# Kernel optimization log

Measured on AMD Instinct MI355X. Metric: run time of the kernel, lower is better.

Reference implementation:

```python
import jax, jax.numpy as jnp
import numpy as np

B, S, H = 16, 2048, 1024
NEG_INF = -10000000.0


def setup_inputs() -> dict:
    key = jax.random.key(0)
    ks = jax.random.split(key, 9)
    s = 1.0 / np.sqrt(H)
    return {
        "queries": jax.random.normal(ks[0], (B, S, H), jnp.float32),
        "keys": jax.random.normal(ks[1], (B, S, H), jnp.float32),
        "values": jax.random.normal(ks[2], (B, S, H), jnp.float32),
        "Wq": jax.random.normal(ks[3], (H, H), jnp.float32) * s,
        "bq": jnp.zeros((H,), jnp.float32),
        "Wk": jax.random.normal(ks[4], (H, H), jnp.float32) * s,
        "bk": jnp.zeros((H,), jnp.float32),
        "Wv": jax.random.normal(ks[5], (H, H), jnp.float32) * s,
        "bv": jnp.zeros((H,), jnp.float32),
    }


def reference(queries, keys, values, Wq, bq, Wk, bk, Wv, bv):
    scale = jax.lax.rsqrt(jnp.float32(H))
    q = jnp.einsum('bsh,oh->bso', queries, Wq) + bq  # (B,S,H)
    k = jnp.einsum('bsh,oh->bso', keys, Wk) + bk
    v = jnp.einsum('bsh,oh->bso', values, Wv) + bv
    scores = jnp.einsum('bqh,bkh->bqk', q, k) * scale  # (B,S,S)
    # Faithful to original: mask = NEG_INF * triu(ones) with diagonal=0,
    # so the diagonal is masked too; softmax over dim=1 (query axis).
    mask = NEG_INF * jnp.triu(jnp.ones((S, S), jnp.float32))
    attn = jax.nn.softmax(scores + mask, axis=1)  # normalize over query dim, as in torch Softmax(dim=1)
    context = jnp.einsum('bqk,bkh->bqh', attn, v)  # (B,S,H)
    return (context, attn)
```

## Files before the change

kernel.cpp:

```cpp
#include <hip/hip_runtime.h>
#include <hip/hip_bf16.h>
#include <stdint.h>

#define B_ 16
#define S_ 2048
#define H_ 1024
static constexpr float NEG_INF_F = -10000000.0f;
static constexpr float SCALE_F   = 0.03125f;

#define BM 256
#define BN 256
#define BK 64
#define HALF_BYTES 16384
#define OPBUF_BYTES 32768

typedef __attribute__((ext_vector_type(4))) float  f32x4;
typedef __attribute__((ext_vector_type(8))) short  bf16x8;
typedef __attribute__((ext_vector_type(4))) short  s16x4;

__device__ __forceinline__ short f2bf(float f) {
  uint32_t u = __float_as_uint(f);
  u = (u + 0x7FFFu + ((u >> 16) & 1u)) >> 16;
  return (short)u;
}

__device__ __forceinline__ void gload16(const void* g, void* l) {
  __builtin_amdgcn_global_load_lds(
      (const __attribute__((address_space(1))) unsigned int*)g,
      (__attribute__((address_space(3))) unsigned int*)l, 16, 0, 0);
}

__device__ __forceinline__ bf16x8 lds_frag(const char* buf, int r, int k) {
  int byte = ((r >> 7) << 14) + ((r & 127) << 7) + (k << 1);
  byte ^= (r & 7) << 4;
  return *(const bf16x8*)(buf + byte);
}

__device__ __forceinline__ void stage_half(const short* __restrict__ rows0,
                                           int ld, int kt, char* dst) {
  const int t = threadIdx.x, w = t >> 6, l = t & 63;
  #pragma unroll
  for (int j = 0; j < 2; ++j) {
    const int idx16 = j * 512 + w * 64 + l;
    const int r  = idx16 >> 3;
    const int cs = ((l & 7) << 4) ^ ((r & 7) << 4);
    gload16(rows0 + (size_t)r * ld + kt + (cs >> 1),
            dst + (size_t)(j * 512 + w * 64) * 16);
  }
}

template<int MODE>
__device__ __forceinline__ void gemm_core256(
    const short* __restrict__ A, const short* __restrict__ Bm,
    const float* __restrict__ bias, void* __restrict__ Cp,
    int K, int lda, int ldb, int ldc, int z, long long strC,
    int row0, int col0, int bx, char* lds) {
  char* ldsA = lds;
  char* ldsB = lds + 2 * OPBUF_BYTES;
  const int lane = threadIdx.x & 63;
  const int wid  = threadIdx.x >> 6;
  const int wm = wid >> 2;
  const int wn = wid & 3;
  const int lr = lane & 15;
  const int lk = (lane >> 4) << 3;

  int kmain = K;
  if constexpr (MODE == 3) { int km = (bx + 1) * BM; kmain = km < K ? km : K; }
  const int ntm = kmain / BK;
  const int nt  = ntm + ((MODE == 3 && kmain < K) ? 1 : 0);

  f32x4 acc[8][4] = {};

  const short* Arows0 = A + (size_t)row0 * lda;
  const short* Arows1 = Arows0 + (size_t)128 * lda;
  const short* Brows0 = Bm + (size_t)col0 * ldb;
  const short* Brows1 = Brows0 + (size_t)128 * ldb;

  auto stage_tile = [&](int buf, int kt) {
    stage_half(Brows0, ldb, kt, ldsB + buf * OPBUF_BYTES);
    stage_half(Brows1, ldb, kt, ldsB + buf * OPBUF_BYTES + HALF_BYTES);
    stage_half(Arows0, lda, kt, ldsA + buf * OPBUF_BYTES);
    stage_half(Arows1, lda, kt, ldsA + buf * OPBUF_BYTES + HALF_BYTES);
  };

  stage_tile(0, 0);
  asm volatile("s_waitcnt vmcnt(0)" ::: "memory");
  __builtin_amdgcn_s_barrier();

  for (int i = 0; i < nt; ++i) {
    const int c = i & 1;
    const char* bA = ldsA + c * OPBUF_BYTES;
    const char* bB = ldsB + c * OPBUF_BYTES;
    if (i + 1 < nt) {
      const int ktn = (i + 1 < ntm) ? (i + 1) * BK : K - BK;
      stage_tile(c ^ 1, ktn);
    }

    bf16x8 bfr[4][2];
    #pragma unroll
    for (int q = 0; q < 4; ++q) {
      if (q == 0) {
        #pragma unroll
        for (int nf = 0; nf < 4; ++nf)
          #pragma unroll
          for (int ks = 0; ks < 2; ++ks)
            bfr[nf][ks] = lds_frag(bB, wn * 64 + nf * 16 + lr, ks * 32 + lk);
      }
      bf16x8 af[2][2];
      #pragma unroll
      for (int fm = 0; fm < 2; ++fm)
        #pragma unroll
        for (int ks = 0; ks < 2; ++ks)
          af[fm][ks] = lds_frag(bA, wm * 128 + q * 32 + fm * 16 + lr, ks * 32 + lk);
      asm volatile("s_waitcnt lgkmcnt(0)" ::: "memory");
      __builtin_amdgcn_sched_barrier(0);
      __builtin_amdgcn_s_setprio(1);
      #pragma unroll
      for (int fm = 0; fm < 2; ++fm)
        #pragma unroll
        for (int nf = 0; nf < 4; ++nf)
          #pragma unroll
          for (int ks = 0; ks < 2; ++ks)
            acc[q * 2 + fm][nf] = __builtin_amdgcn_mfma_f32_16x16x32_bf16(
                af[fm][ks], bfr[nf][ks], acc[q * 2 + fm][nf], 0, 0, 0);
      __builtin_amdgcn_s_setprio(0);
      if (q < 3) __builtin_amdgcn_s_barrier();
    }
    asm volatile("s_waitcnt vmcnt(0)" ::: "memory");
    __builtin_amdgcn_s_barrier();
  }

  #pragma unroll
  for (int mf = 0; mf < 8; ++mf) {
    #pragma unroll
    for (int nf = 0; nf < 4; ++nf) {
      const int mb = row0 + wm * 128 + mf * 16 + ((lane >> 4) << 2);
      const int n  = col0 + wn * 64 + nf * 16 + lr;
      f32x4 a = acc[mf][nf];
      if constexpr (MODE == 0) {
        short* out = (short*)Cp;
        const float bv = bias[n];
        #pragma unroll
        for (int r = 0; r < 4; ++r)
          out[(size_t)(mb + r) * ldc + n] = f2bf(a[r] + bv);
      } else if constexpr (MODE == 1) {
        const float bv = bias[n];
        const int bb = mb >> 11;
        const int ss = mb & (S_ - 1);
        s16x4 pk;
        #pragma unroll
        for (int r = 0; r < 4; ++r) pk[r] = f2bf(a[r] + bv);
        *(s16x4*)((short*)Cp + ((size_t)bb * H_ + n) * S_ + ss) = pk;
      } else if constexpr (MODE == 2) {
        float* out = (float*)Cp + (size_t)z * strC;
        #pragma unroll
        for (int r = 0; r < 4; ++r) {
          const int m = mb + r;
          out[(size_t)m * ldc + n] = a[r] * SCALE_F + (n >= m ? NEG_INF_F : 0.0f);
        }
      } else {
        float* out = (float*)Cp + (size_t)z * strC;
        #pragma unroll
        for (int r = 0; r < 4; ++r)
          out[(size_t)(mb + r) * ldc + n] = a[r];
      }
    }
  }
}

struct ProjArgs {
  const short *xq, *xk, *xv, *wq, *wk, *wv;
  const float *bq, *bk, *bv;
  short *oq, *ok, *ov;
};

__launch_bounds__(512, 1)
__global__ void proj3(ProjArgs p) {
  __shared__ char lds[4 * OPBUF_BYTES];
  const int z = blockIdx.z;
  const int row0 = blockIdx.y * BM;
  const int col0 = blockIdx.x * BN;
  if (z == 0)
    gemm_core256<0>(p.xq, p.wq, p.bq, p.oq, H_, H_, H_, H_, 0, 0LL, row0, col0, blockIdx.x, lds);
  else if (z == 1)
    gemm_core256<0>(p.xk, p.wk, p.bk, p.ok, H_, H_, H_, H_, 0, 0LL, row0, col0, blockIdx.x, lds);
  else
    gemm_core256<1>(p.xv, p.wv, p.bv, p.ov, H_, H_, H_, 0, 0, 0LL, row0, col0, blockIdx.x, lds);
}

__launch_bounds__(512, 1)
__global__ void scores_k(const short* __restrict__ Qb, const short* __restrict__ Kb,
                         float* __restrict__ attn) {
  if (blockIdx.y > blockIdx.x && blockIdx.y != gridDim.y - 1) return;
  __shared__ char lds[4 * OPBUF_BYTES];
  const size_t zo = (size_t)blockIdx.z * S_ * H_;
  gemm_core256<2>(Qb + zo, Kb + zo, nullptr, attn, H_, H_, H_, S_, blockIdx.z,
                  (long long)S_ * S_, blockIdx.x * BM, blockIdx.y * BN, blockIdx.x, lds);
}

__launch_bounds__(512, 1)
__global__ void ctx_k(const short* __restrict__ attn_b, const short* __restrict__ Vt,
                      float* __restrict__ ctx) {
  __shared__ char lds[4 * OPBUF_BYTES];
  gemm_core256<3>(attn_b + (size_t)blockIdx.z * S_ * S_, Vt + (size_t)blockIdx.z * H_ * S_,
                  nullptr, ctx, S_, S_, S_, H_, blockIdx.z, (long long)S_ * H_,
                  blockIdx.x * BM, blockIdx.y * BN, blockIdx.x, lds);
}

__launch_bounds__(256)
__global__ void cvt6(const float* __restrict__ q, const float* __restrict__ k,
                     const float* __restrict__ v, const float* __restrict__ wq,
                     const float* __restrict__ wk, const float* __restrict__ wv,
                     short* __restrict__ xq, short* __restrict__ xk,
                     short* __restrict__ xv, short* __restrict__ wqb,
                     short* __restrict__ wkb, short* __restrict__ wvb) {
  const int y = blockIdx.y;
  const int stride = gridDim.x * 256;
  if (y < 3) {
    const float* s = (y == 0) ? q : (y == 1) ? k : v;
    short* d       = (y == 0) ? xq : (y == 1) ? xk : xv;
    const int n4 = (B_ * S_ * H_) / 4;
    for (int i = blockIdx.x * 256 + threadIdx.x; i < n4; i += stride) {
      f32x4 x = ((const f32x4*)s)[i];
      s16x4 o;
      #pragma unroll
      for (int j = 0; j < 4; ++j) o[j] = f2bf(x[j]);
      ((s16x4*)d)[i] = o;
    }
  } else {
    const int w4 = (H_ * H_) / 4;
    for (int i = blockIdx.x * 256 + threadIdx.x; i < 3 * w4; i += stride) {
      const int wsel = i >> 18;
      const int j = i & (w4 - 1);
      const float* s = (wsel == 0) ? wq : (wsel == 1) ? wk : wv;
      short* d       = (wsel == 0) ? wqb : (wsel == 1) ? wkb : wvb;
      f32x4 x = ((const f32x4*)s)[j];
      s16x4 o;
      #pragma unroll
      for (int jj = 0; jj < 4; ++jj) o[jj] = f2bf(x[jj]);
      ((s16x4*)d)[j] = o;
    }
  }
}

__launch_bounds__(256)
__global__ void softmax_col(float* __restrict__ attn, short* __restrict__ attn_b) {
  const int b  = blockIdx.y;
  const int t  = threadIdx.x;
  const int cg = t & 7;
  const int qo = t >> 3;
  const int k0 = blockIdx.x * 32 + cg * 4;
  float* base = attn + (size_t)b * S_ * S_;
  short* bb   = attn_b + (size_t)b * S_ * S_;
  const bool full = (k0 == S_ - 4);

  int qstart;
  if (full) qstart = qo;
  else { const int s0 = k0 + 1; qstart = s0 + ((qo - s0) & 31); }

  f32x4 m4, s4;
  #pragma unroll
  for (int i = 0; i < 4; ++i) { m4[i] = -3.0e38f; s4[i] = 0.0f; }

  for (int q = qstart; q < S_; q += 32) {
    f32x4 x = *(const f32x4*)&base[(size_t)q * S_ + k0];
    #pragma unroll
    for (int i = 0; i < 4; ++i) {
      float mn = fmaxf(m4[i], x[i]);
      s4[i] = s4[i] * __expf(m4[i] - mn) + __expf(x[i] - mn);
      m4[i] = mn;
    }
  }

  __shared__ f32x4 smx[32][8];
  __shared__ f32x4 ssx[32][8];
  smx[qo][cg] = m4;
  ssx[qo][cg] = s4;
  __syncthreads();

  f32x4 M4, Sm;
  #pragma unroll
  for (int i = 0; i < 4; ++i) { M4[i] = -3.0e38f; Sm[i] = 0.0f; }
  for (int j = 0; j < 32; ++j) {
    f32x4 mm = smx[j][cg];
    #pragma unroll
    for (int i = 0; i < 4; ++i) M4[i] = fmaxf(M4[i], mm[i]);
  }
  for (int j = 0; j < 32; ++j) {
    f32x4 mm = smx[j][cg], ssv = ssx[j][cg];
    #pragma unroll
    for (int i = 0; i < 4; ++i) Sm[i] += ssv[i] * __expf(mm[i] - M4[i]);
  }
  f32x4 inv;
  #pragma unroll
  for (int i = 0; i < 4; ++i) inv[i] = 1.0f / Sm[i];

  for (int q = qo; q < S_; q += 32) {
    const size_t off = (size_t)q * S_ + k0;
    if (full || q > k0) {
      f32x4 x = *(const f32x4*)&base[off];
      f32x4 r;
      s16x4 rb;
      #pragma unroll
      for (int i = 0; i < 4; ++i) { r[i] = __expf(x[i] - M4[i]) * inv[i]; rb[i] = f2bf(r[i]); }
      *(f32x4*)&base[off] = r;
      *(s16x4*)&bb[off]   = rb;
    } else {
      f32x4 zr;
      s16x4 zb;
      #pragma unroll
      for (int i = 0; i < 4; ++i) { zr[i] = 0.0f; zb[i] = 0; }
      *(f32x4*)&base[off] = zr;
      *(s16x4*)&bb[off]   = zb;
    }
  }
}

extern "C" void kernel_launch(void* const* d_in, const int* in_sizes, int n_in,
                              void* d_out, int out_size, void* d_ws, size_t ws_size,
                              hipStream_t stream) {
  const float* queries = (const float*)d_in[0];
  const float* keys    = (const float*)d_in[1];
  const float* values  = (const float*)d_in[2];
  const float* Wq = (const float*)d_in[3];
  const float* bq = (const float*)d_in[4];
  const float* Wk = (const float*)d_in[5];
  const float* bk = (const float*)d_in[6];
  const float* Wv = (const float*)d_in[7];
  const float* bv = (const float*)d_in[8];

  float* ctx  = (float*)d_out;
  float* attn = ctx + (size_t)B_ * S_ * H_;

  short* Qb = (short*)d_ws;
  short* Kb = Qb + (size_t)B_ * S_ * H_;
  short* Vt = Kb + (size_t)B_ * S_ * H_;
  short* attn_b = Qb;

  short* Wqb = (short*)ctx;
  short* Wkb = Wqb + (size_t)H_ * H_;
  short* Wvb = Wkb + (size_t)H_ * H_;
  short* Xq = (short*)attn;
  short* Xk = Xq + (size_t)B_ * S_ * H_;
  short* Xv = Xk + (size_t)B_ * S_ * H_;

  cvt6<<<dim3(2048, 4, 1), dim3(256, 1, 1), 0, stream>>>(queries, keys, values,
                                                         Wq, Wk, Wv,
                                                         Xq, Xk, Xv, Wqb, Wkb, Wvb);

  ProjArgs pa{Xq, Xk, Xv, Wqb, Wkb, Wvb, bq, bk, bv, Qb, Kb, Vt};
  proj3<<<dim3(H_ / BN, 32768 / BM, 3), dim3(512, 1, 1), 0, stream>>>(pa);

  scores_k<<<dim3(S_ / BM, S_ / BN, B_), dim3(512, 1, 1), 0, stream>>>(Qb, Kb, attn);

  softmax_col<<<dim3(S_ / 32, B_, 1), dim3(256, 1, 1), 0, stream>>>(attn, attn_b);

  ctx_k<<<dim3(S_ / BM, H_ / BN, B_), dim3(512, 1, 1), 0, stream>>>(attn_b, Vt, ctx);
}
```

Baseline: 894.1 us.

## Fuse column softmax statistics into scores GEMM epilogue and remap block order

The scores GEMM epilogue now computes per-column running max and sum-of-exp for its 256-row tile, reduces them across lanes and waves, and writes float2 partials to a scratch buffer. The softmax kernel then merges these 8 partials per column instead of doing a full read pass over the fp32 attention matrix. This removes one full read of the large scores buffer. Separately, all three GEMM kernels remap block IDs, likely so each group of 8 consecutive block IDs lands on tiles that share inputs in cache. The cost is extra exp work and an LDS reduction in the GEMM epilogue, plus a dependency on scratch space carved out of the ctx output region.

After: 828.6 us. 1.08x faster.

```diff
diff --git a/kernel.cpp b/kernel.cpp
--- a/kernel.cpp
+++ b/kernel.cpp
@@ -54,7 +54,7 @@
     const short* __restrict__ A, const short* __restrict__ Bm,
     const float* __restrict__ bias, void* __restrict__ Cp,
     int K, int lda, int ldb, int ldc, int z, long long strC,
-    int row0, int col0, int bx, char* lds) {
+    int row0, int col0, int bx, char* lds, float2* __restrict__ partials) {
   char* ldsA = lds;
   char* ldsB = lds + 2 * OPBUF_BYTES;
   const int lane = threadIdx.x & 63;
@@ -130,6 +130,8 @@
     __builtin_amdgcn_s_barrier();
   }
 
+  float pm[4] = {-3.0e38f, -3.0e38f, -3.0e38f, -3.0e38f};
+
   #pragma unroll
   for (int mf = 0; mf < 8; ++mf) {
     #pragma unroll
@@ -155,8 +157,10 @@
         float* out = (float*)Cp + (size_t)z * strC;
         #pragma unroll
         for (int r = 0; r < 4; ++r) {
-          const int m = mb + r;
-          out[(size_t)m * ldc + n] = a[r] * SCALE_F + (n >= m ? NEG_INF_F : 0.0f);
+          const int mrow = mb + r;
+          float v = a[r] * SCALE_F + (n >= mrow ? NEG_INF_F : 0.0f);
+          out[(size_t)mrow * ldc + n] = v;
+          pm[nf] = fmaxf(pm[nf], v);
         }
       } else {
         float* out = (float*)Cp + (size_t)z * strC;
@@ -164,6 +168,51 @@
         for (int r = 0; r < 4; ++r)
           out[(size_t)(mb + r) * ldc + n] = a[r];
       }
+    }
+  }
+
+  if constexpr (MODE == 2) {
+    float ps[4] = {0.0f, 0.0f, 0.0f, 0.0f};
+    #pragma unroll
+    for (int mf = 0; mf < 8; ++mf)
+      #pragma unroll
+      for (int nf = 0; nf < 4; ++nf) {
+        const int mb = row0 + wm * 128 + mf * 16 + ((lane >> 4) << 2);
+        const int n  = col0 + wn * 64 + nf * 16 + lr;
+        f32x4 a = acc[mf][nf];
+        #pragma unroll
+        for (int r = 0; r < 4; ++r) {
+          float v = a[r] * SCALE_F + (n >= mb + r ? NEG_INF_F : 0.0f);
+          ps[nf] += __expf(v - pm[nf]);
+        }
+      }
+    float* smx = (float*)lds;
+    float* sse = smx + 512;
+    #pragma unroll
+    for (int nf = 0; nf < 4; ++nf) {
+      float m = pm[nf], s = ps[nf];
+      #pragma unroll
+      for (int d = 16; d < 64; d <<= 1) {
+        float om = __shfl_xor(m, d);
+        float os = __shfl_xor(s, d);
+        float nm = fmaxf(m, om);
+        s = s * __expf(m - nm) + os * __expf(om - nm);
+        m = nm;
+      }
+      if ((lane >> 4) == 0) {
+        smx[wm * 256 + wn * 64 + nf * 16 + lr] = m;
+        sse[wm * 256 + wn * 64 + nf * 16 + lr] = s;
+      }
+    }
+    __syncthreads();
+    if (threadIdx.x < 256) {
+      const int col = threadIdx.x;
+      float m0 = smx[col], m1 = smx[256 + col];
+      float s0 = sse[col], s1 = sse[256 + col];
+      float mm = fmaxf(m0, m1);
+      float ss = s0 * __expf(m0 - mm) + s1 * __expf(m1 - mm);
+      float2 pv; pv.x = mm; pv.y = ss;
+      partials[((size_t)z * 8 + (row0 >> 8)) * S_ + col0 + col] = pv;
     }
   }
 }
@@ -177,34 +226,48 @@
 __launch_bounds__(512, 1)
 __global__ void proj3(ProjArgs p) {
   __shared__ char lds[4 * OPBUF_BYTES];
-  const int z = blockIdx.z;
-  const int row0 = blockIdx.y * BM;
-  const int col0 = blockIdx.x * BN;
+  const int bid = blockIdx.x + (blockIdx.y << 2) + (blockIdx.z << 9);
+  const int s = (bid & 7) * 192 + (bid >> 3);
+  const int z = s >> 9;
+  const int y = (s & 511) >> 2;
+  const int x = s & 3;
+  const int row0 = y * BM;
+  const int col0 = x * BN;
   if (z == 0)
-    gemm_core256<0>(p.xq, p.wq, p.bq, p.oq, H_, H_, H_, H_, 0, 0LL, row0, col0, blockIdx.x, lds);
+    gemm_core256<0>(p.xq, p.wq, p.bq, p.oq, H_, H_, H_, H_, 0, 0LL, row0, col0, x, lds, nullptr);
   else if (z == 1)
-    gemm_core256<0>(p.xk, p.wk, p.bk, p.ok, H_, H_, H_, H_, 0, 0LL, row0, col0, blockIdx.x, lds);
+    gemm_core256<0>(p.xk, p.wk, p.bk, p.ok, H_, H_, H_, H_, 0, 0LL, row0, col0, x, lds, nullptr);
   else
-    gemm_core256<1>(p.xv, p.wv, p.bv, p.ov, H_, H_, H_, 0, 0, 0LL, row0, col0, blockIdx.x, lds);
+    gemm_core256<1>(p.xv, p.wv, p.bv, p.ov, H_, H_, H_, 0, 0, 0LL, row0, col0, x, lds, nullptr);
 }
 
 __launch_bounds__(512, 1)
 __global__ void scores_k(const short* __restrict__ Qb, const short* __restrict__ Kb,
-                         float* __restrict__ attn) {
-  if (blockIdx.y > blockIdx.x && blockIdx.y != gridDim.y - 1) return;
+                         float* __restrict__ attn, float2* __restrict__ partials) {
+  const int bid = blockIdx.x + (blockIdx.y << 3) + (blockIdx.z << 6);
+  const int s = (bid & 7) * 128 + (bid >> 3);
+  const int bz = s >> 6;
+  const int by = (s >> 3) & 7;
+  const int bx = s & 7;
+  if (by > bx && by != 7) return;
   __shared__ char lds[4 * OPBUF_BYTES];
-  const size_t zo = (size_t)blockIdx.z * S_ * H_;
-  gemm_core256<2>(Qb + zo, Kb + zo, nullptr, attn, H_, H_, H_, S_, blockIdx.z,
-                  (long long)S_ * S_, blockIdx.x * BM, blockIdx.y * BN, blockIdx.x, lds);
+  const size_t zo = (size_t)bz * S_ * H_;
+  gemm_core256<2>(Qb + zo, Kb + zo, nullptr, attn, H_, H_, H_, S_, bz,
+                  (long long)S_ * S_, bx * BM, by * BN, bx, lds, partials);
 }
 
 __launch_bounds__(512, 1)
 __global__ void ctx_k(const short* __restrict__ attn_b, const short* __restrict__ Vt,
                       float* __restrict__ ctx) {
+  const int bid = blockIdx.x + (blockIdx.y << 3) + (blockIdx.z << 5);
+  const int s = (bid & 7) * 64 + (bid >> 3);
+  const int bz = s >> 5;
+  const int by = (s >> 3) & 3;
+  const int bx = s & 7;
   __shared__ char lds[4 * OPBUF_BYTES];
-  gemm_core256<3>(attn_b + (size_t)blockIdx.z * S_ * S_, Vt + (size_t)blockIdx.z * H_ * S_,
-                  nullptr, ctx, S_, S_, S_, H_, blockIdx.z, (long long)S_ * H_,
-                  blockIdx.x * BM, blockIdx.y * BN, blockIdx.x, lds);
+  gemm_core256<3>(attn_b + (size_t)bz * S_ * S_, Vt + (size_t)bz * H_ * S_,
+                  nullptr, ctx, S_, S_, S_, H_, bz, (long long)S_ * H_,
+                  bx * BM, by * BN, bx, lds, nullptr);
 }
 
 __launch_bounds__(256)
@@ -244,7 +307,8 @@
 }
 
 __launch_bounds__(256)
-__global__ void softmax_col(float* __restrict__ attn, short* __restrict__ attn_b) {
+__global__ void softmax_col(float* __restrict__ attn, short* __restrict__ attn_b,
+                            const float2* __restrict__ partials) {
   const int b  = blockIdx.y;
   const int t  = threadIdx.x;
   const int cg = t & 7;
@@ -254,46 +318,32 @@
   short* bb   = attn_b + (size_t)b * S_ * S_;
   const bool full = (k0 == S_ - 4);
 
-  int qstart;
-  if (full) qstart = qo;
-  else { const int s0 = k0 + 1; qstart = s0 + ((qo - s0) & 31); }
-
-  f32x4 m4, s4;
-  #pragma unroll
-  for (int i = 0; i < 4; ++i) { m4[i] = -3.0e38f; s4[i] = 0.0f; }
-
-  for (int q = qstart; q < S_; q += 32) {
-    f32x4 x = *(const f32x4*)&base[(size_t)q * S_ + k0];
-    #pragma unroll
-    for (int i = 0; i < 4; ++i) {
-      float mn = fmaxf(m4[i], x[i]);
-      s4[i] = s4[i] * __expf(m4[i] - mn) + __expf(x[i] - mn);
-      m4[i] = mn;
-    }
-  }
-
-  __shared__ f32x4 smx[32][8];
-  __shared__ f32x4 ssx[32][8];
-  smx[qo][cg] = m4;
-  ssx[qo][cg] = s4;
+  __shared__ f32x4 bM[8], bI[8];
+  if (qo == 0) {
+    const int by = k0 >> 8;
+    const int bxlo = (by == 7) ? 0 : by;
+    f32x4 M4, Sm;
+    #pragma unroll
+    for (int i = 0; i < 4; ++i) { M4[i] = -3.0e38f; Sm[i] = 0.0f; }
+    for (int bx = bxlo; bx < 8; ++bx) {
+      const float2* p = partials + ((size_t)b * 8 + bx) * S_ + k0;
+      #pragma unroll
+      for (int i = 0; i < 4; ++i) {
+        float2 pv = p[i];
+        float nm = fmaxf(M4[i], pv.x);
+        Sm[i] = Sm[i] * __expf(M4[i] - nm) + pv.y * __expf(pv.x - nm);
+        M4[i] = nm;
+      }
+    }
+    f32x4 inv;
+    #pragma unroll
+    for (int i = 0; i < 4; ++i) inv[i] = 1.0f / Sm[i];
+    bM[cg] = M4;
+    bI[cg] = inv;
+  }
   __syncthreads();
-
-  f32x4 M4, Sm;
-  #pragma unroll
-  for (int i = 0; i < 4; ++i) { M4[i] = -3.0e38f; Sm[i] = 0.0f; }
-  for (int j = 0; j < 32; ++j) {
-    f32x4 mm = smx[j][cg];
-    #pragma unroll
-    for (int i = 0; i < 4; ++i) M4[i] = fmaxf(M4[i], mm[i]);
-  }
-  for (int j = 0; j < 32; ++j) {
-    f32x4 mm = smx[j][cg], ssv = ssx[j][cg];
-    #pragma unroll
-    for (int i = 0; i < 4; ++i) Sm[i] += ssv[i] * __expf(mm[i] - M4[i]);
-  }
-  f32x4 inv;
-  #pragma unroll
-  for (int i = 0; i < 4; ++i) inv[i] = 1.0f / Sm[i];
+  const f32x4 M4  = bM[cg];
+  const f32x4 inv = bI[cg];
 
   for (int q = qo; q < S_; q += 32) {
     const size_t off = (size_t)q * S_ + k0;
@@ -340,6 +390,7 @@
   short* Wqb = (short*)ctx;
   short* Wkb = Wqb + (size_t)H_ * H_;
   short* Wvb = Wkb + (size_t)H_ * H_;
+  float2* partials = (float2*)(Wvb + (size_t)H_ * H_);
   short* Xq = (short*)attn;
   short* Xk = Xq + (size_t)B_ * S_ * H_;
   short* Xv = Xk + (size_t)B_ * S_ * H_;
@@ -351,9 +402,9 @@
   ProjArgs pa{Xq, Xk, Xv, Wqb, Wkb, Wvb, bq, bk, bv, Qb, Kb, Vt};
   proj3<<<dim3(H_ / BN, 32768 / BM, 3), dim3(512, 1, 1), 0, stream>>>(pa);
 
-  scores_k<<<dim3(S_ / BM, S_ / BN, B_), dim3(512, 1, 1), 0, stream>>>(Qb, Kb, attn);
-
-  softmax_col<<<dim3(S_ / 32, B_, 1), dim3(256, 1, 1), 0, stream>>>(attn, attn_b);
+  scores_k<<<dim3(S_ / BM, S_ / BN, B_), dim3(512, 1, 1), 0, stream>>>(Qb, Kb, attn, partials);
+
+  softmax_col<<<dim3(S_ / 32, B_, 1), dim3(256, 1, 1), 0, stream>>>(attn, attn_b, partials);
 
   ctx_k<<<dim3(S_ / BM, H_ / BN, B_), dim3(512, 1, 1), 0, stream>>>(attn_b, Vt, ctx);
 }
```
